# Kernel tuning notes

Hardware: AMD Instinct MI355X
Metric: run time of the kernel (lower is better)

Reference implementation:

```python
import jax, jax.numpy as jnp
import numpy as np

BATCH, IN_DIM, HID, OUT_DIM = 8192, 128, 1024, 128
W_SCALE = 0.05  # keep tanh out of saturation, like xavier init


def setup_inputs() -> dict:
    key = jax.random.key(0)
    k = jax.random.split(key, 5)
    return {
        "u": jax.random.normal(k[0], (BATCH, IN_DIM), dtype=jnp.float32),
        "B_w": jax.random.normal(k[1], (HID, IN_DIM), dtype=jnp.float32) * W_SCALE,
        "Bs_full": jax.random.normal(k[2], (HID, HID), dtype=jnp.float32) * W_SCALE,
        "Ds_w": jax.random.normal(k[3], (OUT_DIM, HID), dtype=jnp.float32) * W_SCALE,
        "D_w": jax.random.normal(k[4], (OUT_DIM, IN_DIM), dtype=jnp.float32) * W_SCALE,
    }


def reference(u, B_w, Bs_full, Ds_w, D_w):
    # s_i = tanh( sum_{j<i} Bs[i,j] * s_j + (B u)_i ),  y = Ds s + D u
    H = Bs_full.shape[0]
    Bs = jnp.tril(Bs_full, k=-1)          # strictly lower triangular [H, H]
    Bu = u @ B_w.T                        # [B, H]
    s0 = jnp.zeros_like(Bu)               # state buffer; entries >= i are 0,
                                          # so using the full masked row of Bs
                                          # equals the j<i partial sum.

    def step(s, xs):
        row, bu_i, i = xs                 # row: [H], bu_i: [B], i: scalar
        s_i = jnp.tanh(s @ row + bu_i)    # [B]
        return s.at[:, i].set(s_i), None

    s, _ = jax.lax.scan(step, s0, (Bs, Bu.T, jnp.arange(H)))
    return s @ Ds_w.T + u @ D_w.T         # [B, OUT_DIM]
```

## Files before the change

### kernel.cpp

```cpp
#include <hip/hip_runtime.h>

typedef unsigned short u16;
typedef __attribute__((ext_vector_type(8))) short bfrag;
typedef __attribute__((ext_vector_type(4))) float f32x4;

#define SROW 1032

__device__ __forceinline__ u16 f2bf(float x) {
    unsigned int v = __float_as_uint(x);
    return (u16)((v + 0x7FFFu + ((v >> 16) & 1u)) >> 16);
}

__device__ __forceinline__ float fast_tanh(float x) {
    float e = __builtin_amdgcn_exp2f(x * 2.885390081777927f);
    return __builtin_fmaf(-2.0f, __builtin_amdgcn_rcpf(e + 1.0f), 1.0f);
}

__global__ void ren_prologue(const float* __restrict__ Bs, const float* __restrict__ Bw,
                             const float* __restrict__ Ds, const float* __restrict__ Dw,
                             u16* __restrict__ bs16, u16* __restrict__ bw16,
                             u16* __restrict__ ds16, u16* __restrict__ dw16,
                             float* __restrict__ diagT)
{
    const int g = blockIdx.x * 256 + threadIdx.x;
    if (g < 262144) {
        const int idx = g * 4;
        const int i = idx >> 10, j = idx & 1023;
        const float4 v = *reinterpret_cast<const float4*>(Bs + idx);
        u16 o[4];
        o[0] = (j + 0 < i) ? f2bf(v.x) : (u16)0;
        o[1] = (j + 1 < i) ? f2bf(v.y) : (u16)0;
        o[2] = (j + 2 < i) ? f2bf(v.z) : (u16)0;
        o[3] = (j + 3 < i) ? f2bf(v.w) : (u16)0;
        *reinterpret_cast<uint2*>(bs16 + idx) = *reinterpret_cast<const uint2*>(o);
    } else if (g < 294912) {
        const int idx = (g - 262144) * 4;
        const float4 v = *reinterpret_cast<const float4*>(Bw + idx);
        u16 o[4] = { f2bf(v.x), f2bf(v.y), f2bf(v.z), f2bf(v.w) };
        *reinterpret_cast<uint2*>(bw16 + idx) = *reinterpret_cast<const uint2*>(o);
    } else if (g < 327680) {
        const int idx = (g - 294912) * 4;
        const float4 v = *reinterpret_cast<const float4*>(Ds + idx);
        u16 o[4] = { f2bf(v.x), f2bf(v.y), f2bf(v.z), f2bf(v.w) };
        *reinterpret_cast<uint2*>(ds16 + idx) = *reinterpret_cast<const uint2*>(o);
    } else if (g < 331776) {
        const int idx = (g - 327680) * 4;
        const float4 v = *reinterpret_cast<const float4*>(Dw + idx);
        u16 o[4] = { f2bf(v.x), f2bf(v.y), f2bf(v.z), f2bf(v.w) };
        *reinterpret_cast<uint2*>(dw16 + idx) = *reinterpret_cast<const uint2*>(o);
    } else if (g < 339968) {
        const int lin0 = (g - 331776) * 4;
        #pragma unroll
        for (int t = 0; t < 4; ++t) {
            const int l = lin0 + t;
            const int bb = l >> 10, rem = l & 1023, i = rem >> 5, j = rem & 31;
            diagT[l] = (j > i) ? Bs[(size_t)(bb * 32 + j) * 1024 + (bb * 32 + i)] : 0.0f;
        }
    }
}

__global__ __launch_bounds__(192) void ren_main(
    const float* __restrict__ u,
    const u16* __restrict__ bs16, const u16* __restrict__ bw16,
    const u16* __restrict__ ds16, const u16* __restrict__ dw16,
    const float* __restrict__ diagT,
    float* __restrict__ out)
{
    __shared__ __align__(16) u16   sh_S[32 * SROW];
    __shared__ __align__(16) float sh_acc[32 * 36];
    __shared__ __align__(16) float sh_dT[2][1024];

    const int tid  = threadIdx.x;
    const int wave = tid >> 6;
    const int lane = tid & 63;
    const int mt   = wave;
    const int lr   = lane & 15;
    const int lk8  = (lane >> 4) << 3;
    const int row0 = blockIdx.x << 5;

    bfrag fu[4];
    f32x4 accA0, accA1;

    if (wave < 2) {
        const float* up = u + (size_t)(row0 + mt * 16 + lr) * 128 + lk8;
        #pragma unroll
        for (int kk = 0; kk < 4; ++kk) {
            float4 a = *reinterpret_cast<const float4*>(up + kk * 32);
            float4 c = *reinterpret_cast<const float4*>(up + kk * 32 + 4);
            bfrag f;
            f[0] = (short)f2bf(a.x); f[1] = (short)f2bf(a.y);
            f[2] = (short)f2bf(a.z); f[3] = (short)f2bf(a.w);
            f[4] = (short)f2bf(c.x); f[5] = (short)f2bf(c.y);
            f[6] = (short)f2bf(c.z); f[7] = (short)f2bf(c.w);
            fu[kk] = f;
        }
        {
            const float4* g = reinterpret_cast<const float4*>(diagT + tid * 8);
            float4 a = g[0], c = g[1];
            *reinterpret_cast<float4*>(&sh_dT[0][tid * 8])     = a;
            *reinterpret_cast<float4*>(&sh_dT[0][tid * 8 + 4]) = c;
        }
        accA0 = (f32x4){0.f,0.f,0.f,0.f}; accA1 = (f32x4){0.f,0.f,0.f,0.f};
        const u16* p0 = bw16 + (size_t)(lr)      * 128 + lk8;
        const u16* p1 = bw16 + (size_t)(16 + lr) * 128 + lk8;
        #pragma unroll
        for (int kk = 0; kk < 4; ++kk) {
            accA0 = __builtin_amdgcn_mfma_f32_16x16x32_bf16(fu[kk], *reinterpret_cast<const bfrag*>(p0 + kk * 32), accA0, 0, 0, 0);
            accA1 = __builtin_amdgcn_mfma_f32_16x16x32_bf16(fu[kk], *reinterpret_cast<const bfrag*>(p1 + kk * 32), accA1, 0, 0, 0);
        }
        const int m = (mt << 4) + ((lane >> 4) << 2);
        #pragma unroll
        for (int rr = 0; rr < 4; ++rr) {
            sh_acc[(m + rr) * 36 + lr]      = accA0[rr];
            sh_acc[(m + rr) * 36 + 16 + lr] = accA1[rr];
        }
    }
    __syncthreads();

    for (int b = 0; b < 32; ++b) {
        if (wave == 2) {
            if (lane < 32) {
                float part[32];
                const float* accr = sh_acc + lane * 36;
                #pragma unroll
                for (int q = 0; q < 8; ++q) {
                    float4 v = reinterpret_cast<const float4*>(accr)[q];
                    part[4*q+0] = v.x; part[4*q+1] = v.y; part[4*q+2] = v.z; part[4*q+3] = v.w;
                }
                const float4* dT4 = reinterpret_cast<const float4*>(&sh_dT[b & 1][0]);
                float4 wreg[3][8];
                #pragma unroll
                for (int q = 0; q < 8; ++q) wreg[0][q] = dT4[q];
                #pragma unroll
                for (int q = 0; q < 8; ++q) wreg[1][q] = dT4[8 + q];
                u16* srow = sh_S + lane * SROW + (b << 5);
                u16 sv[8];
                #pragma unroll
                for (int i = 0; i < 32; ++i) {
                    if (i + 2 < 32) {
                        #pragma unroll
                        for (int q = (i + 3) >> 2; q < 8; ++q)
                            wreg[(i + 2) % 3][q] = dT4[((i + 2) << 3) + q];
                    }
                    float s = fast_tanh(part[i]);
                    sv[i & 7] = (u16)((__float_as_uint(s) + 0x8000u) >> 16);
                    if ((i & 7) == 7) {
                        uint4 pk;
                        pk.x = (unsigned)sv[0] | ((unsigned)sv[1] << 16);
                        pk.y = (unsigned)sv[2] | ((unsigned)sv[3] << 16);
                        pk.z = (unsigned)sv[4] | ((unsigned)sv[5] << 16);
                        pk.w = (unsigned)sv[6] | ((unsigned)sv[7] << 16);
                        *reinterpret_cast<uint4*>(srow + ((i >> 3) << 3)) = pk;
                    }
                    #pragma unroll
                    for (int q = (i + 1) >> 2; q < 8; ++q) {
                        float4 w = wreg[i % 3][q];
                        part[4*q+0] = __builtin_fmaf(w.x, s, part[4*q+0]);
                        part[4*q+1] = __builtin_fmaf(w.y, s, part[4*q+1]);
                        part[4*q+2] = __builtin_fmaf(w.z, s, part[4*q+2]);
                        part[4*q+3] = __builtin_fmaf(w.w, s, part[4*q+3]);
                    }
                }
            }
        } else if (b < 31) {
            const int nb = b + 1;
            const float4* g = reinterpret_cast<const float4*>(diagT + (nb << 10) + tid * 8);
            float4 st0 = g[0], st1 = g[1];

            accA0 = (f32x4){0.f,0.f,0.f,0.f}; accA1 = (f32x4){0.f,0.f,0.f,0.f};
            const u16* p0 = bw16 + (size_t)((nb << 5) + lr)      * 128 + lk8;
            const u16* p1 = bw16 + (size_t)((nb << 5) + 16 + lr) * 128 + lk8;
            #pragma unroll
            for (int kk = 0; kk < 4; ++kk) {
                accA0 = __builtin_amdgcn_mfma_f32_16x16x32_bf16(fu[kk], *reinterpret_cast<const bfrag*>(p0 + kk * 32), accA0, 0, 0, 0);
                accA1 = __builtin_amdgcn_mfma_f32_16x16x32_bf16(fu[kk], *reinterpret_cast<const bfrag*>(p1 + kk * 32), accA1, 0, 0, 0);
            }
            const u16* bsp0 = bs16 + (size_t)((nb << 5) + lr)      * 1024 + lk8;
            const u16* bsp1 = bs16 + (size_t)((nb << 5) + 16 + lr) * 1024 + lk8;
            const u16* ssp  = sh_S + ((mt << 4) + lr) * SROW + lk8;
            #pragma unroll 8
            for (int kc = 0; kc < b; ++kc) {
                bfrag af = *reinterpret_cast<const bfrag*>(ssp + (kc << 5));
                accA0 = __builtin_amdgcn_mfma_f32_16x16x32_bf16(af, *reinterpret_cast<const bfrag*>(bsp0 + (kc << 5)), accA0, 0, 0, 0);
                accA1 = __builtin_amdgcn_mfma_f32_16x16x32_bf16(af, *reinterpret_cast<const bfrag*>(bsp1 + (kc << 5)), accA1, 0, 0, 0);
            }
            *reinterpret_cast<float4*>(&sh_dT[nb & 1][tid * 8])     = st0;
            *reinterpret_cast<float4*>(&sh_dT[nb & 1][tid * 8 + 4]) = st1;
        }
        __syncthreads();

        if (wave < 2 && b < 31) {
            const int nb = b + 1;
            const u16* bsp0 = bs16 + (size_t)((nb << 5) + lr)      * 1024 + lk8;
            const u16* bsp1 = bs16 + (size_t)((nb << 5) + 16 + lr) * 1024 + lk8;
            const u16* ssp  = sh_S + ((mt << 4) + lr) * SROW + lk8;
            bfrag af = *reinterpret_cast<const bfrag*>(ssp + (b << 5));
            accA0 = __builtin_amdgcn_mfma_f32_16x16x32_bf16(af, *reinterpret_cast<const bfrag*>(bsp0 + (b << 5)), accA0, 0, 0, 0);
            accA1 = __builtin_amdgcn_mfma_f32_16x16x32_bf16(af, *reinterpret_cast<const bfrag*>(bsp1 + (b << 5)), accA1, 0, 0, 0);
            const int m = (mt << 4) + ((lane >> 4) << 2);
            #pragma unroll
            for (int rr = 0; rr < 4; ++rr) {
                sh_acc[(m + rr) * 36 + lr]      = accA0[rr];
                sh_acc[(m + rr) * 36 + 16 + lr] = accA1[rr];
            }
        }
        __syncthreads();
    }

    if (wave >= 2) return;

    f32x4 ey[8];
    #pragma unroll
    for (int t = 0; t < 8; ++t) ey[t] = (f32x4){0.f,0.f,0.f,0.f};

    const u16* ssp = sh_S + ((mt << 4) + lr) * SROW + lk8;
    #pragma unroll 2
    for (int kc = 0; kc < 32; ++kc) {
        bfrag af = *reinterpret_cast<const bfrag*>(ssp + (kc << 5));
        #pragma unroll
        for (int t = 0; t < 8; ++t) {
            bfrag bf = *reinterpret_cast<const bfrag*>(ds16 + (size_t)(t * 16 + lr) * 1024 + (kc << 5) + lk8);
            ey[t] = __builtin_amdgcn_mfma_f32_16x16x32_bf16(af, bf, ey[t], 0, 0, 0);
        }
    }
    #pragma unroll
    for (int kk = 0; kk < 4; ++kk) {
        #pragma unroll
        for (int t = 0; t < 8; ++t) {
            bfrag bf = *reinterpret_cast<const bfrag*>(dw16 + (t * 16 + lr) * 128 + (kk << 5) + lk8);
            ey[t] = __builtin_amdgcn_mfma_f32_16x16x32_bf16(fu[kk], bf, ey[t], 0, 0, 0);
        }
    }
    {
        const int mbase = row0 + (mt << 4) + ((lane >> 4) << 2);
        #pragma unroll
        for (int t = 0; t < 8; ++t) {
            #pragma unroll
            for (int rr = 0; rr < 4; ++rr)
                out[(size_t)(mbase + rr) * 128 + t * 16 + lr] = ey[t][rr];
        }
    }
}

extern "C" void kernel_launch(void* const* d_in, const int* in_sizes, int n_in,
                              void* d_out, int out_size, void* d_ws, size_t ws_size,
                              hipStream_t stream)
{
    const float* u  = (const float*)d_in[0];
    const float* Bw = (const float*)d_in[1];
    const float* Bs = (const float*)d_in[2];
    const float* Ds = (const float*)d_in[3];
    const float* Dw = (const float*)d_in[4];
    float* out = (float*)d_out;

    u16* bs16 = (u16*)d_ws;
    u16* bw16 = bs16 + 1024 * 1024;
    u16* ds16 = bw16 + 1024 * 128;
    u16* dw16 = ds16 + 128 * 1024;
    float* diagT = (float*)(dw16 + 128 * 128);

    ren_prologue<<<1328, 256, 0, stream>>>(Bs, Bw, Ds, Dw, bs16, bw16, ds16, dw16, diagT);
    ren_main<<<256, 192, 0, stream>>>(u, bs16, bw16, ds16, dw16, diagT, out);
}
```

Measured before the change: 190.0 us.

## Halve recurrence block size to 16 and split serial tanh across two lane halves

The sequential block width drops from 32 to 16 (64 blocks), so each serial triangular solve step does half the dependent FMA chain, and the MFMA waves use one 16-wide tile per block. The serial wave now uses all 64 lanes: lanes 0-15 and 16-31 each run a duplicated pA/pB chain, and the selected result is written to sh_S with scalar stores. sh_S is zero-filled with one extra padding row for lanes beyond 32. The aim is to shorten the critical path of the recurrence, at the cost of twice as many barriers and block iterations and less MFMA work per sync.

```diff
diff --git a/kernel.cpp b/kernel.cpp
--- a/kernel.cpp
+++ b/kernel.cpp
@@ -5,6 +5,8 @@
 typedef __attribute__((ext_vector_type(4))) float f32x4;
 
 #define SROW 1032
+#define NBLK 64
+#define ACCW 20
 
 __device__ __forceinline__ u16 f2bf(float x) {
     unsigned int v = __float_as_uint(x);
@@ -48,13 +50,13 @@
         const float4 v = *reinterpret_cast<const float4*>(Dw + idx);
         u16 o[4] = { f2bf(v.x), f2bf(v.y), f2bf(v.z), f2bf(v.w) };
         *reinterpret_cast<uint2*>(dw16 + idx) = *reinterpret_cast<const uint2*>(o);
-    } else if (g < 339968) {
+    } else if (g < 335872) {
         const int lin0 = (g - 331776) * 4;
         #pragma unroll
         for (int t = 0; t < 4; ++t) {
             const int l = lin0 + t;
-            const int bb = l >> 10, rem = l & 1023, i = rem >> 5, j = rem & 31;
-            diagT[l] = (j > i) ? Bs[(size_t)(bb * 32 + j) * 1024 + (bb * 32 + i)] : 0.0f;
+            const int bb = l >> 8, rem = l & 255, i = rem >> 4, j = rem & 15;
+            diagT[l] = (j > i) ? Bs[(size_t)(bb * 16 + j) * 1024 + (bb * 16 + i)] : 0.0f;
         }
     }
 }
@@ -66,9 +68,9 @@
     const float* __restrict__ diagT,
     float* __restrict__ out)
 {
-    __shared__ __align__(16) u16   sh_S[32 * SROW];
-    __shared__ __align__(16) float sh_acc[32 * 36];
-    __shared__ __align__(16) float sh_dT[2][1024];
+    __shared__ __align__(16) u16   sh_S[33 * SROW];
+    __shared__ __align__(16) float sh_acc[32 * ACCW];
+    __shared__ __align__(16) float sh_dT[2][256];
 
     const int tid  = threadIdx.x;
     const int wave = tid >> 6;
@@ -78,8 +80,11 @@
     const int lk8  = (lane >> 4) << 3;
     const int row0 = blockIdx.x << 5;
 
+    for (int e = tid * 8; e < 33 * SROW; e += 192 * 8)
+        *reinterpret_cast<uint4*>(sh_S + e) = (uint4){0u, 0u, 0u, 0u};
+
     bfrag fu[4];
-    f32x4 accA0, accA1;
+    f32x4 acc;
 
     if (wave < 2) {
         const float* up = u + (size_t)(row0 + mt * 16 + lr) * 128 + lk8;
@@ -94,115 +99,100 @@
             f[6] = (short)f2bf(c.z); f[7] = (short)f2bf(c.w);
             fu[kk] = f;
         }
-        {
-            const float4* g = reinterpret_cast<const float4*>(diagT + tid * 8);
-            float4 a = g[0], c = g[1];
-            *reinterpret_cast<float4*>(&sh_dT[0][tid * 8])     = a;
-            *reinterpret_cast<float4*>(&sh_dT[0][tid * 8 + 4]) = c;
-        }
-        accA0 = (f32x4){0.f,0.f,0.f,0.f}; accA1 = (f32x4){0.f,0.f,0.f,0.f};
-        const u16* p0 = bw16 + (size_t)(lr)      * 128 + lk8;
-        const u16* p1 = bw16 + (size_t)(16 + lr) * 128 + lk8;
-        #pragma unroll
-        for (int kk = 0; kk < 4; ++kk) {
-            accA0 = __builtin_amdgcn_mfma_f32_16x16x32_bf16(fu[kk], *reinterpret_cast<const bfrag*>(p0 + kk * 32), accA0, 0, 0, 0);
-            accA1 = __builtin_amdgcn_mfma_f32_16x16x32_bf16(fu[kk], *reinterpret_cast<const bfrag*>(p1 + kk * 32), accA1, 0, 0, 0);
-        }
+        if (tid < 128) {
+            float2 d0 = reinterpret_cast<const float2*>(diagT)[tid];
+            reinterpret_cast<float2*>(&sh_dT[0][0])[tid] = d0;
+        }
+        acc = (f32x4){0.f, 0.f, 0.f, 0.f};
+        const u16* p0 = bw16 + (size_t)lr * 128 + lk8;
+        #pragma unroll
+        for (int kk = 0; kk < 4; ++kk)
+            acc = __builtin_amdgcn_mfma_f32_16x16x32_bf16(fu[kk], *reinterpret_cast<const bfrag*>(p0 + kk * 32), acc, 0, 0, 0);
         const int m = (mt << 4) + ((lane >> 4) << 2);
         #pragma unroll
-        for (int rr = 0; rr < 4; ++rr) {
-            sh_acc[(m + rr) * 36 + lr]      = accA0[rr];
-            sh_acc[(m + rr) * 36 + 16 + lr] = accA1[rr];
-        }
+        for (int rr = 0; rr < 4; ++rr)
+            sh_acc[(m + rr) * ACCW + lr] = acc[rr];
     }
     __syncthreads();
 
-    for (int b = 0; b < 32; ++b) {
+    for (int b = 0; b < NBLK; ++b) {
         if (wave == 2) {
-            if (lane < 32) {
-                float part[32];
-                const float* accr = sh_acc + lane * 36;
+            const float* accr = sh_acc + (lane & 31) * ACCW;
+            float pA[16], pB[16];
+            #pragma unroll
+            for (int q = 0; q < 4; ++q) {
+                float4 v = reinterpret_cast<const float4*>(accr)[q];
+                pA[4*q+0] = v.x; pA[4*q+1] = v.y; pA[4*q+2] = v.z; pA[4*q+3] = v.w;
+                pB[4*q+0] = v.x; pB[4*q+1] = v.y; pB[4*q+2] = v.z; pB[4*q+3] = v.w;
+            }
+            const float4* dT4 = reinterpret_cast<const float4*>(&sh_dT[b & 1][0]);
+            float4 wreg[3][4];
+            #pragma unroll
+            for (int q = 0; q < 4; ++q) wreg[0][q] = dT4[q];
+            #pragma unroll
+            for (int q = 0; q < 4; ++q) wreg[1][q] = dT4[4 + q];
+            const bool isA = (lane < 16);
+            u16* srow = sh_S + min(lane, 32) * SROW + (b << 4);
+            #pragma unroll
+            for (int i = 0; i < 16; ++i) {
+                if (i + 2 < 16) {
+                    #pragma unroll
+                    for (int q = (i + 3) >> 2; q < 4; ++q)
+                        wreg[(i + 2) % 3][q] = dT4[((i + 2) << 2) + q];
+                }
+                float sA = fast_tanh(pA[i]);
+                float sB = fast_tanh(pB[i]);
+                float ss = isA ? sA : sB;
+                srow[i] = (u16)((__float_as_uint(ss) + 0x8000u) >> 16);
                 #pragma unroll
-                for (int q = 0; q < 8; ++q) {
-                    float4 v = reinterpret_cast<const float4*>(accr)[q];
-                    part[4*q+0] = v.x; part[4*q+1] = v.y; part[4*q+2] = v.z; part[4*q+3] = v.w;
-                }
-                const float4* dT4 = reinterpret_cast<const float4*>(&sh_dT[b & 1][0]);
-                float4 wreg[3][8];
-                #pragma unroll
-                for (int q = 0; q < 8; ++q) wreg[0][q] = dT4[q];
-                #pragma unroll
-                for (int q = 0; q < 8; ++q) wreg[1][q] = dT4[8 + q];
-                u16* srow = sh_S + lane * SROW + (b << 5);
-                u16 sv[8];
-                #pragma unroll
-                for (int i = 0; i < 32; ++i) {
-                    if (i + 2 < 32) {
-                        #pragma unroll
-                        for (int q = (i + 3) >> 2; q < 8; ++q)
-                            wreg[(i + 2) % 3][q] = dT4[((i + 2) << 3) + q];
-                    }
-                    float s = fast_tanh(part[i]);
-                    sv[i & 7] = (u16)((__float_as_uint(s) + 0x8000u) >> 16);
-                    if ((i & 7) == 7) {
-                        uint4 pk;
-                        pk.x = (unsigned)sv[0] | ((unsigned)sv[1] << 16);
-                        pk.y = (unsigned)sv[2] | ((unsigned)sv[3] << 16);
-                        pk.z = (unsigned)sv[4] | ((unsigned)sv[5] << 16);
-                        pk.w = (unsigned)sv[6] | ((unsigned)sv[7] << 16);
-                        *reinterpret_cast<uint4*>(srow + ((i >> 3) << 3)) = pk;
-                    }
-                    #pragma unroll
-                    for (int q = (i + 1) >> 2; q < 8; ++q) {
-                        float4 w = wreg[i % 3][q];
-                        part[4*q+0] = __builtin_fmaf(w.x, s, part[4*q+0]);
-                        part[4*q+1] = __builtin_fmaf(w.y, s, part[4*q+1]);
-                        part[4*q+2] = __builtin_fmaf(w.z, s, part[4*q+2]);
-                        part[4*q+3] = __builtin_fmaf(w.w, s, part[4*q+3]);
-                    }
+                for (int q = (i + 1) >> 2; q < 4; ++q) {
+                    float4 w = wreg[i % 3][q];
+                    pA[4*q+0] = __builtin_fmaf(w.x, sA, pA[4*q+0]);
+                    pA[4*q+1] = __builtin_fmaf(w.y, sA, pA[4*q+1]);
+                    pA[4*q+2] = __builtin_fmaf(w.z, sA, pA[4*q+2]);
+                    pA[4*q+3] = __builtin_fmaf(w.w, sA, pA[4*q+3]);
+                    pB[4*q+0] = __builtin_fmaf(w.x, sB, pB[4*q+0]);
+                    pB[4*q+1] = __builtin_fmaf(w.y, sB, pB[4*q+1]);
+                    pB[4*q+2] = __builtin_fmaf(w.z, sB, pB[4*q+2]);
+                    pB[4*q+3] = __builtin_fmaf(w.w, sB, pB[4*q+3]);
                 }
             }
-        } else if (b < 31) {
-            const int nb = b + 1;
-            const float4* g = reinterpret_cast<const float4*>(diagT + (nb << 10) + tid * 8);
-            float4 st0 = g[0], st1 = g[1];
-
-            accA0 = (f32x4){0.f,0.f,0.f,0.f}; accA1 = (f32x4){0.f,0.f,0.f,0.f};
-            const u16* p0 = bw16 + (size_t)((nb << 5) + lr)      * 128 + lk8;
-            const u16* p1 = bw16 + (size_t)((nb << 5) + 16 + lr) * 128 + lk8;
-            #pragma unroll
-            for (int kk = 0; kk < 4; ++kk) {
-                accA0 = __builtin_amdgcn_mfma_f32_16x16x32_bf16(fu[kk], *reinterpret_cast<const bfrag*>(p0 + kk * 32), accA0, 0, 0, 0);
-                accA1 = __builtin_amdgcn_mfma_f32_16x16x32_bf16(fu[kk], *reinterpret_cast<const bfrag*>(p1 + kk * 32), accA1, 0, 0, 0);
+        }
+
+        bfrag bfin;
+        const int nb = b + 1;
+        const int tf = b >> 1;
+        if (wave < 2 && b < NBLK - 1) {
+            float2 dstage;
+            if (tid < 128) dstage = reinterpret_cast<const float2*>(diagT + (nb << 8))[tid];
+            bfin = *reinterpret_cast<const bfrag*>(bs16 + (size_t)((nb << 4) + lr) * 1024 + (tf << 5) + lk8);
+
+            acc = (f32x4){0.f, 0.f, 0.f, 0.f};
+            const u16* p0 = bw16 + (size_t)((nb << 4) + lr) * 128 + lk8;
+            #pragma unroll
+            for (int kk = 0; kk < 4; ++kk)
+                acc = __builtin_amdgcn_mfma_f32_16x16x32_bf16(fu[kk], *reinterpret_cast<const bfrag*>(p0 + kk * 32), acc, 0, 0, 0);
+
+            const u16* bsp = bs16 + (size_t)((nb << 4) + lr) * 1024 + lk8;
+            const u16* ssp = sh_S + ((mt << 4) + lr) * SROW + lk8;
+            const int npart = b >> 1;
+            #pragma unroll 8
+            for (int t = 0; t < npart; ++t) {
+                bfrag af = *reinterpret_cast<const bfrag*>(ssp + (t << 5));
+                acc = __builtin_amdgcn_mfma_f32_16x16x32_bf16(af, *reinterpret_cast<const bfrag*>(bsp + (t << 5)), acc, 0, 0, 0);
             }
-            const u16* bsp0 = bs16 + (size_t)((nb << 5) + lr)      * 1024 + lk8;
-            const u16* bsp1 = bs16 + (size_t)((nb << 5) + 16 + lr) * 1024 + lk8;
-            const u16* ssp  = sh_S + ((mt << 4) + lr) * SROW + lk8;
-            #pragma unroll 8
-            for (int kc = 0; kc < b; ++kc) {
-                bfrag af = *reinterpret_cast<const bfrag*>(ssp + (kc << 5));
-                accA0 = __builtin_amdgcn_mfma_f32_16x16x32_bf16(af, *reinterpret_cast<const bfrag*>(bsp0 + (kc << 5)), accA0, 0, 0, 0);
-                accA1 = __builtin_amdgcn_mfma_f32_16x16x32_bf16(af, *reinterpret_cast<const bfrag*>(bsp1 + (kc << 5)), accA1, 0, 0, 0);
-            }
-            *reinterpret_cast<float4*>(&sh_dT[nb & 1][tid * 8])     = st0;
-            *reinterpret_cast<float4*>(&sh_dT[nb & 1][tid * 8 + 4]) = st1;
+            if (tid < 128) reinterpret_cast<float2*>(&sh_dT[nb & 1][0])[tid] = dstage;
         }
         __syncthreads();
 
-        if (wave < 2 && b < 31) {
-            const int nb = b + 1;
-            const u16* bsp0 = bs16 + (size_t)((nb << 5) + lr)      * 1024 + lk8;
-            const u16* bsp1 = bs16 + (size_t)((nb << 5) + 16 + lr) * 1024 + lk8;
-            const u16* ssp  = sh_S + ((mt << 4) + lr) * SROW + lk8;
-            bfrag af = *reinterpret_cast<const bfrag*>(ssp + (b << 5));
-            accA0 = __builtin_amdgcn_mfma_f32_16x16x32_bf16(af, *reinterpret_cast<const bfrag*>(bsp0 + (b << 5)), accA0, 0, 0, 0);
-            accA1 = __builtin_amdgcn_mfma_f32_16x16x32_bf16(af, *reinterpret_cast<const bfrag*>(bsp1 + (b << 5)), accA1, 0, 0, 0);
+        if (wave < 2 && b < NBLK - 1) {
+            const u16* ssp = sh_S + ((mt << 4) + lr) * SROW + lk8;
+            bfrag af = *reinterpret_cast<const bfrag*>(ssp + (tf << 5));
+            acc = __builtin_amdgcn_mfma_f32_16x16x32_bf16(af, bfin, acc, 0, 0, 0);
             const int m = (mt << 4) + ((lane >> 4) << 2);
             #pragma unroll
-            for (int rr = 0; rr < 4; ++rr) {
-                sh_acc[(m + rr) * 36 + lr]      = accA0[rr];
-                sh_acc[(m + rr) * 36 + 16 + lr] = accA1[rr];
-            }
+            for (int rr = 0; rr < 4; ++rr)
+                sh_acc[(m + rr) * ACCW + lr] = acc[rr];
         }
         __syncthreads();
     }
@@ -211,7 +201,7 @@
 
     f32x4 ey[8];
     #pragma unroll
-    for (int t = 0; t < 8; ++t) ey[t] = (f32x4){0.f,0.f,0.f,0.f};
+    for (int t = 0; t < 8; ++t) ey[t] = (f32x4){0.f, 0.f, 0.f, 0.f};
 
     const u16* ssp = sh_S + ((mt << 4) + lr) * SROW + lk8;
     #pragma unroll 2
@@ -259,6 +249,6 @@
     u16* dw16 = ds16 + 128 * 1024;
     float* diagT = (float*)(dw16 + 128 * 128);
 
-    ren_prologue<<<1328, 256, 0, stream>>>(Bs, Bw, Ds, Dw, bs16, bw16, ds16, dw16, diagT);
+    ren_prologue<<<1312, 256, 0, stream>>>(Bs, Bw, Ds, Dw, bs16, bw16, ds16, dw16, diagT);
     ren_main<<<256, 192, 0, stream>>>(u, bs16, bw16, ds16, dw16, diagT, out);
 }
```

Result: slower. 257.5 us (+35.5%).

## Collapse ren_main to single-wave blocks of 16 rows, removing barriers

Applied to the files above, without the earlier changes.

The 3-wave block (two MFMA waves plus one scalar tanh-recurrence wave over 32 rows) becomes one 64-lane wave that handles 16 rows, with 512 blocks instead of 256. The same wave does the serial within-block recurrence and then the MFMA accumulation for the next block, so all __syncthreads go away and the grid gets more, smaller blocks. In exchange, the recurrence and the MFMA work no longer overlap inside a block and only 16 lanes are active during the scalar phase. Overlap now has to come from several resident blocks per CU, which the smaller LDS footprint should allow.

```diff
diff --git a/kernel.cpp b/kernel.cpp
--- a/kernel.cpp
+++ b/kernel.cpp
@@ -5,6 +5,7 @@
 typedef __attribute__((ext_vector_type(4))) float f32x4;
 
 #define SROW 1032
+#define ACCW 36
 
 __device__ __forceinline__ u16 f2bf(float x) {
     unsigned int v = __float_as_uint(x);
@@ -59,30 +60,25 @@
     }
 }
 
-__global__ __launch_bounds__(192) void ren_main(
+__global__ __launch_bounds__(64) void ren_main(
     const float* __restrict__ u,
     const u16* __restrict__ bs16, const u16* __restrict__ bw16,
     const u16* __restrict__ ds16, const u16* __restrict__ dw16,
     const float* __restrict__ diagT,
     float* __restrict__ out)
 {
-    __shared__ __align__(16) u16   sh_S[32 * SROW];
-    __shared__ __align__(16) float sh_acc[32 * 36];
+    __shared__ __align__(16) u16   sh_S[16 * SROW];
+    __shared__ __align__(16) float sh_acc[16 * ACCW];
     __shared__ __align__(16) float sh_dT[2][1024];
 
-    const int tid  = threadIdx.x;
-    const int wave = tid >> 6;
-    const int lane = tid & 63;
-    const int mt   = wave;
+    const int lane = threadIdx.x;
     const int lr   = lane & 15;
     const int lk8  = (lane >> 4) << 3;
-    const int row0 = blockIdx.x << 5;
+    const int row0 = blockIdx.x << 4;
 
     bfrag fu[4];
-    f32x4 accA0, accA1;
-
-    if (wave < 2) {
-        const float* up = u + (size_t)(row0 + mt * 16 + lr) * 128 + lk8;
+    {
+        const float* up = u + (size_t)(row0 + lr) * 128 + lk8;
         #pragma unroll
         for (int kk = 0; kk < 4; ++kk) {
             float4 a = *reinterpret_cast<const float4*>(up + kk * 32);
@@ -94,126 +90,133 @@
             f[6] = (short)f2bf(c.z); f[7] = (short)f2bf(c.w);
             fu[kk] = f;
         }
-        {
-            const float4* g = reinterpret_cast<const float4*>(diagT + tid * 8);
-            float4 a = g[0], c = g[1];
-            *reinterpret_cast<float4*>(&sh_dT[0][tid * 8])     = a;
-            *reinterpret_cast<float4*>(&sh_dT[0][tid * 8 + 4]) = c;
-        }
-        accA0 = (f32x4){0.f,0.f,0.f,0.f}; accA1 = (f32x4){0.f,0.f,0.f,0.f};
-        const u16* p0 = bw16 + (size_t)(lr)      * 128 + lk8;
+    }
+
+    float4 st[4];
+    f32x4 acc0, acc1;
+    float part[32];
+
+    {
+        const float4* g = reinterpret_cast<const float4*>(diagT);
+        #pragma unroll
+        for (int t = 0; t < 4; ++t) st[t] = g[4 * lane + t];
+        float4* dd = reinterpret_cast<float4*>(&sh_dT[0][0]);
+        #pragma unroll
+        for (int t = 0; t < 4; ++t) dd[4 * lane + t] = st[t];
+
+        acc0 = (f32x4){0.f,0.f,0.f,0.f}; acc1 = (f32x4){0.f,0.f,0.f,0.f};
+        const u16* p0 = bw16 + (size_t)lr * 128 + lk8;
         const u16* p1 = bw16 + (size_t)(16 + lr) * 128 + lk8;
         #pragma unroll
         for (int kk = 0; kk < 4; ++kk) {
-            accA0 = __builtin_amdgcn_mfma_f32_16x16x32_bf16(fu[kk], *reinterpret_cast<const bfrag*>(p0 + kk * 32), accA0, 0, 0, 0);
-            accA1 = __builtin_amdgcn_mfma_f32_16x16x32_bf16(fu[kk], *reinterpret_cast<const bfrag*>(p1 + kk * 32), accA1, 0, 0, 0);
-        }
-        const int m = (mt << 4) + ((lane >> 4) << 2);
+            acc0 = __builtin_amdgcn_mfma_f32_16x16x32_bf16(fu[kk], *reinterpret_cast<const bfrag*>(p0 + kk * 32), acc0, 0, 0, 0);
+            acc1 = __builtin_amdgcn_mfma_f32_16x16x32_bf16(fu[kk], *reinterpret_cast<const bfrag*>(p1 + kk * 32), acc1, 0, 0, 0);
+        }
+        const int m = (lane >> 4) << 2;
         #pragma unroll
         for (int rr = 0; rr < 4; ++rr) {
-            sh_acc[(m + rr) * 36 + lr]      = accA0[rr];
-            sh_acc[(m + rr) * 36 + 16 + lr] = accA1[rr];
-        }
-    }
-    __syncthreads();
+            sh_acc[(m + rr) * ACCW + lr]      = acc0[rr];
+            sh_acc[(m + rr) * ACCW + 16 + lr] = acc1[rr];
+        }
+        if (lane < 16) {
+            const float4* ar = reinterpret_cast<const float4*>(sh_acc + lane * ACCW);
+            #pragma unroll
+            for (int q = 0; q < 8; ++q) {
+                float4 v = ar[q];
+                part[4*q+0] = v.x; part[4*q+1] = v.y; part[4*q+2] = v.z; part[4*q+3] = v.w;
+            }
+        }
+    }
 
     for (int b = 0; b < 32; ++b) {
-        if (wave == 2) {
-            if (lane < 32) {
-                float part[32];
-                const float* accr = sh_acc + lane * 36;
+        const int nb = b + 1;
+        if (nb < 32) {
+            const float4* g = reinterpret_cast<const float4*>(diagT + (nb << 10));
+            #pragma unroll
+            for (int t = 0; t < 4; ++t) st[t] = g[4 * lane + t];
+        }
+
+        if (lane < 16) {
+            const float4* dT4 = reinterpret_cast<const float4*>(&sh_dT[b & 1][0]);
+            float4 wreg[3][8];
+            #pragma unroll
+            for (int q = 0; q < 8; ++q) wreg[0][q] = dT4[q];
+            #pragma unroll
+            for (int q = 0; q < 8; ++q) wreg[1][q] = dT4[8 + q];
+            u16* srow = sh_S + lane * SROW + (b << 5);
+            u16 sv[8];
+            #pragma unroll
+            for (int i = 0; i < 32; ++i) {
+                if (i + 2 < 32) {
+                    #pragma unroll
+                    for (int q = (i + 3) >> 2; q < 8; ++q)
+                        wreg[(i + 2) % 3][q] = dT4[((i + 2) << 3) + q];
+                }
+                float s = fast_tanh(part[i]);
+                sv[i & 7] = (u16)((__float_as_uint(s) + 0x8000u) >> 16);
+                if ((i & 7) == 7) {
+                    uint4 pk;
+                    pk.x = (unsigned)sv[0] | ((unsigned)sv[1] << 16);
+                    pk.y = (unsigned)sv[2] | ((unsigned)sv[3] << 16);
+                    pk.z = (unsigned)sv[4] | ((unsigned)sv[5] << 16);
+                    pk.w = (unsigned)sv[6] | ((unsigned)sv[7] << 16);
+                    *reinterpret_cast<uint4*>(srow + ((i >> 3) << 3)) = pk;
+                }
+                #pragma unroll
+                for (int q = (i + 1) >> 2; q < 8; ++q) {
+                    float4 w = wreg[i % 3][q];
+                    part[4*q+0] = __builtin_fmaf(w.x, s, part[4*q+0]);
+                    part[4*q+1] = __builtin_fmaf(w.y, s, part[4*q+1]);
+                    part[4*q+2] = __builtin_fmaf(w.z, s, part[4*q+2]);
+                    part[4*q+3] = __builtin_fmaf(w.w, s, part[4*q+3]);
+                }
+            }
+        }
+
+        if (nb < 32) {
+            float4* dd = reinterpret_cast<float4*>(&sh_dT[nb & 1][0]);
+            #pragma unroll
+            for (int t = 0; t < 4; ++t) dd[4 * lane + t] = st[t];
+
+            acc0 = (f32x4){0.f,0.f,0.f,0.f}; acc1 = (f32x4){0.f,0.f,0.f,0.f};
+            const u16* q0 = bw16 + (size_t)((nb << 5) + lr) * 128 + lk8;
+            const u16* q1 = bw16 + (size_t)((nb << 5) + 16 + lr) * 128 + lk8;
+            #pragma unroll
+            for (int kk = 0; kk < 4; ++kk) {
+                acc0 = __builtin_amdgcn_mfma_f32_16x16x32_bf16(fu[kk], *reinterpret_cast<const bfrag*>(q0 + kk * 32), acc0, 0, 0, 0);
+                acc1 = __builtin_amdgcn_mfma_f32_16x16x32_bf16(fu[kk], *reinterpret_cast<const bfrag*>(q1 + kk * 32), acc1, 0, 0, 0);
+            }
+            const u16* bsp0 = bs16 + (size_t)((nb << 5) + lr) * 1024 + lk8;
+            const u16* bsp1 = bs16 + (size_t)((nb << 5) + 16 + lr) * 1024 + lk8;
+            const u16* ssp  = sh_S + lr * SROW + lk8;
+            #pragma unroll 8
+            for (int kc = 0; kc <= b; ++kc) {
+                bfrag af = *reinterpret_cast<const bfrag*>(ssp + (kc << 5));
+                acc0 = __builtin_amdgcn_mfma_f32_16x16x32_bf16(af, *reinterpret_cast<const bfrag*>(bsp0 + (kc << 5)), acc0, 0, 0, 0);
+                acc1 = __builtin_amdgcn_mfma_f32_16x16x32_bf16(af, *reinterpret_cast<const bfrag*>(bsp1 + (kc << 5)), acc1, 0, 0, 0);
+            }
+            const int m = (lane >> 4) << 2;
+            #pragma unroll
+            for (int rr = 0; rr < 4; ++rr) {
+                sh_acc[(m + rr) * ACCW + lr]      = acc0[rr];
+                sh_acc[(m + rr) * ACCW + 16 + lr] = acc1[rr];
+            }
+            if (lane < 16) {
+                const float4* ar = reinterpret_cast<const float4*>(sh_acc + lane * ACCW);
                 #pragma unroll
                 for (int q = 0; q < 8; ++q) {
-                    float4 v = reinterpret_cast<const float4*>(accr)[q];
+                    float4 v = ar[q];
                     part[4*q+0] = v.x; part[4*q+1] = v.y; part[4*q+2] = v.z; part[4*q+3] = v.w;
                 }
-                const float4* dT4 = reinterpret_cast<const float4*>(&sh_dT[b & 1][0]);
-                float4 wreg[3][8];
-                #pragma unroll
-                for (int q = 0; q < 8; ++q) wreg[0][q] = dT4[q];
-                #pragma unroll
-                for (int q = 0; q < 8; ++q) wreg[1][q] = dT4[8 + q];
-                u16* srow = sh_S + lane * SROW + (b << 5);
-                u16 sv[8];
-                #pragma unroll
-                for (int i = 0; i < 32; ++i) {
-                    if (i + 2 < 32) {
-                        #pragma unroll
-                        for (int q = (i + 3) >> 2; q < 8; ++q)
-                            wreg[(i + 2) % 3][q] = dT4[((i + 2) << 3) + q];
-                    }
-                    float s = fast_tanh(part[i]);
-                    sv[i & 7] = (u16)((__float_as_uint(s) + 0x8000u) >> 16);
-                    if ((i & 7) == 7) {
-                        uint4 pk;
-                        pk.x = (unsigned)sv[0] | ((unsigned)sv[1] << 16);
-                        pk.y = (unsigned)sv[2] | ((unsigned)sv[3] << 16);
-                        pk.z = (unsigned)sv[4] | ((unsigned)sv[5] << 16);
-                        pk.w = (unsigned)sv[6] | ((unsigned)sv[7] << 16);
-                        *reinterpret_cast<uint4*>(srow + ((i >> 3) << 3)) = pk;
-                    }
-                    #pragma unroll
-                    for (int q = (i + 1) >> 2; q < 8; ++q) {
-                        float4 w = wreg[i % 3][q];
-                        part[4*q+0] = __builtin_fmaf(w.x, s, part[4*q+0]);
-                        part[4*q+1] = __builtin_fmaf(w.y, s, part[4*q+1]);
-                        part[4*q+2] = __builtin_fmaf(w.z, s, part[4*q+2]);
-                        part[4*q+3] = __builtin_fmaf(w.w, s, part[4*q+3]);
-                    }
-                }
-            }
-        } else if (b < 31) {
-            const int nb = b + 1;
-            const float4* g = reinterpret_cast<const float4*>(diagT + (nb << 10) + tid * 8);
-            float4 st0 = g[0], st1 = g[1];
-
-            accA0 = (f32x4){0.f,0.f,0.f,0.f}; accA1 = (f32x4){0.f,0.f,0.f,0.f};
-            const u16* p0 = bw16 + (size_t)((nb << 5) + lr)      * 128 + lk8;
-            const u16* p1 = bw16 + (size_t)((nb << 5) + 16 + lr) * 128 + lk8;
-            #pragma unroll
-            for (int kk = 0; kk < 4; ++kk) {
-                accA0 = __builtin_amdgcn_mfma_f32_16x16x32_bf16(fu[kk], *reinterpret_cast<const bfrag*>(p0 + kk * 32), accA0, 0, 0, 0);
-                accA1 = __builtin_amdgcn_mfma_f32_16x16x32_bf16(fu[kk], *reinterpret_cast<const bfrag*>(p1 + kk * 32), accA1, 0, 0, 0);
-            }
-            const u16* bsp0 = bs16 + (size_t)((nb << 5) + lr)      * 1024 + lk8;
-            const u16* bsp1 = bs16 + (size_t)((nb << 5) + 16 + lr) * 1024 + lk8;
-            const u16* ssp  = sh_S + ((mt << 4) + lr) * SROW + lk8;
-            #pragma unroll 8
-            for (int kc = 0; kc < b; ++kc) {
-                bfrag af = *reinterpret_cast<const bfrag*>(ssp + (kc << 5));
-                accA0 = __builtin_amdgcn_mfma_f32_16x16x32_bf16(af, *reinterpret_cast<const bfrag*>(bsp0 + (kc << 5)), accA0, 0, 0, 0);
-                accA1 = __builtin_amdgcn_mfma_f32_16x16x32_bf16(af, *reinterpret_cast<const bfrag*>(bsp1 + (kc << 5)), accA1, 0, 0, 0);
-            }
-            *reinterpret_cast<float4*>(&sh_dT[nb & 1][tid * 8])     = st0;
-            *reinterpret_cast<float4*>(&sh_dT[nb & 1][tid * 8 + 4]) = st1;
-        }
-        __syncthreads();
-
-        if (wave < 2 && b < 31) {
-            const int nb = b + 1;
-            const u16* bsp0 = bs16 + (size_t)((nb << 5) + lr)      * 1024 + lk8;
-            const u16* bsp1 = bs16 + (size_t)((nb << 5) + 16 + lr) * 1024 + lk8;
-            const u16* ssp  = sh_S + ((mt << 4) + lr) * SROW + lk8;
-            bfrag af = *reinterpret_cast<const bfrag*>(ssp + (b << 5));
-            accA0 = __builtin_amdgcn_mfma_f32_16x16x32_bf16(af, *reinterpret_cast<const bfrag*>(bsp0 + (b << 5)), accA0, 0, 0, 0);
-            accA1 = __builtin_amdgcn_mfma_f32_16x16x32_bf16(af, *reinterpret_cast<const bfrag*>(bsp1 + (b << 5)), accA1, 0, 0, 0);
-            const int m = (mt << 4) + ((lane >> 4) << 2);
-            #pragma unroll
-            for (int rr = 0; rr < 4; ++rr) {
-                sh_acc[(m + rr) * 36 + lr]      = accA0[rr];
-                sh_acc[(m + rr) * 36 + 16 + lr] = accA1[rr];
-            }
-        }
-        __syncthreads();
-    }
-
-    if (wave >= 2) return;
+            }
+        }
+    }
 
     f32x4 ey[8];
     #pragma unroll
     for (int t = 0; t < 8; ++t) ey[t] = (f32x4){0.f,0.f,0.f,0.f};
 
-    const u16* ssp = sh_S + ((mt << 4) + lr) * SROW + lk8;
+    const u16* ssp = sh_S + lr * SROW + lk8;
     #pragma unroll 2
     for (int kc = 0; kc < 32; ++kc) {
         bfrag af = *reinterpret_cast<const bfrag*>(ssp + (kc << 5));
@@ -232,7 +235,7 @@
         }
     }
     {
-        const int mbase = row0 + (mt << 4) + ((lane >> 4) << 2);
+        const int mbase = row0 + ((lane >> 4) << 2);
         #pragma unroll
         for (int t = 0; t < 8; ++t) {
             #pragma unroll
@@ -260,5 +263,5 @@
     float* diagT = (float*)(dw16 + 128 * 128);
 
     ren_prologue<<<1328, 256, 0, stream>>>(Bs, Bw, Ds, Dw, bs16, bw16, ds16, dw16, diagT);
-    ren_main<<<256, 192, 0, stream>>>(u, bs16, bw16, ds16, dw16, diagT, out);
-}
+    ren_main<<<512, 64, 0, stream>>>(u, bs16, bw16, ds16, dw16, diagT, out);
+}
```

Measured after the change: 235.1 us. 23.8% more time.

## Split MFMA work across four waves per tile and prefetch diagonal Bs fragment

Applied to the files above, without the earlier changes.

Each block now runs four MFMA waves plus one scalar wave instead of two plus one. Each MFMA wave owns a 16x16 quadrant (m-tile, n-tile) rather than a 16x32 strip, which halves the serial MFMA chain per wave in the off-diagonal accumulation, the Bu projection and the output projection. The diagonal Bs fragment for the post-barrier MFMA is loaded before the barrier so that global load leaves the critical path. Scheduling barriers are added in the scalar tanh recurrence to pin instruction order. In exchange the block uses more waves and registers, and each wave reissues the u fragment loads.

```diff
diff --git a/kernel.cpp b/kernel.cpp
--- a/kernel.cpp
+++ b/kernel.cpp
@@ -5,6 +5,7 @@
 typedef __attribute__((ext_vector_type(4))) float f32x4;
 
 #define SROW 1032
+#define ACCW 36
 
 __device__ __forceinline__ u16 f2bf(float x) {
     unsigned int v = __float_as_uint(x);
@@ -59,7 +60,7 @@
     }
 }
 
-__global__ __launch_bounds__(192) void ren_main(
+__global__ __launch_bounds__(320) void ren_main(
     const float* __restrict__ u,
     const u16* __restrict__ bs16, const u16* __restrict__ bw16,
     const u16* __restrict__ ds16, const u16* __restrict__ dw16,
@@ -67,21 +68,22 @@
     float* __restrict__ out)
 {
     __shared__ __align__(16) u16   sh_S[32 * SROW];
-    __shared__ __align__(16) float sh_acc[32 * 36];
+    __shared__ __align__(16) float sh_acc[32 * ACCW];
     __shared__ __align__(16) float sh_dT[2][1024];
 
     const int tid  = threadIdx.x;
     const int wave = tid >> 6;
     const int lane = tid & 63;
-    const int mt   = wave;
+    const int mt   = (wave >> 1) & 1;
+    const int nt   = wave & 1;
     const int lr   = lane & 15;
     const int lk8  = (lane >> 4) << 3;
     const int row0 = blockIdx.x << 5;
 
     bfrag fu[4];
-    f32x4 accA0, accA1;
-
-    if (wave < 2) {
+    f32x4 acc;
+
+    if (wave < 4) {
         const float* up = u + (size_t)(row0 + mt * 16 + lr) * 128 + lk8;
         #pragma unroll
         for (int kk = 0; kk < 4; ++kk) {
@@ -94,45 +96,44 @@
             f[6] = (short)f2bf(c.z); f[7] = (short)f2bf(c.w);
             fu[kk] = f;
         }
-        {
-            const float4* g = reinterpret_cast<const float4*>(diagT + tid * 8);
-            float4 a = g[0], c = g[1];
+        if (tid < 128) {
+            const float4* g = reinterpret_cast<const float4*>(diagT);
+            float4 a = g[2 * tid], c = g[2 * tid + 1];
             *reinterpret_cast<float4*>(&sh_dT[0][tid * 8])     = a;
             *reinterpret_cast<float4*>(&sh_dT[0][tid * 8 + 4]) = c;
         }
-        accA0 = (f32x4){0.f,0.f,0.f,0.f}; accA1 = (f32x4){0.f,0.f,0.f,0.f};
-        const u16* p0 = bw16 + (size_t)(lr)      * 128 + lk8;
-        const u16* p1 = bw16 + (size_t)(16 + lr) * 128 + lk8;
-        #pragma unroll
-        for (int kk = 0; kk < 4; ++kk) {
-            accA0 = __builtin_amdgcn_mfma_f32_16x16x32_bf16(fu[kk], *reinterpret_cast<const bfrag*>(p0 + kk * 32), accA0, 0, 0, 0);
-            accA1 = __builtin_amdgcn_mfma_f32_16x16x32_bf16(fu[kk], *reinterpret_cast<const bfrag*>(p1 + kk * 32), accA1, 0, 0, 0);
-        }
+        acc = (f32x4){0.f, 0.f, 0.f, 0.f};
+        const u16* p0 = bw16 + (size_t)((nt << 4) + lr) * 128 + lk8;
+        #pragma unroll
+        for (int kk = 0; kk < 4; ++kk)
+            acc = __builtin_amdgcn_mfma_f32_16x16x32_bf16(fu[kk], *reinterpret_cast<const bfrag*>(p0 + kk * 32), acc, 0, 0, 0);
         const int m = (mt << 4) + ((lane >> 4) << 2);
         #pragma unroll
-        for (int rr = 0; rr < 4; ++rr) {
-            sh_acc[(m + rr) * 36 + lr]      = accA0[rr];
-            sh_acc[(m + rr) * 36 + 16 + lr] = accA1[rr];
-        }
+        for (int rr = 0; rr < 4; ++rr)
+            sh_acc[(m + rr) * ACCW + (nt << 4) + lr] = acc[rr];
     }
     __syncthreads();
 
     for (int b = 0; b < 32; ++b) {
-        if (wave == 2) {
+        bfrag bfin;
+        const int nb = b + 1;
+
+        if (wave == 4) {
             if (lane < 32) {
+                const float4* dT4 = reinterpret_cast<const float4*>(&sh_dT[b & 1][0]);
+                float4 wreg[3][8];
+                #pragma unroll
+                for (int q = 0; q < 8; ++q) wreg[0][q] = dT4[q];
+                #pragma unroll
+                for (int q = 0; q < 8; ++q) wreg[1][q] = dT4[8 + q];
                 float part[32];
-                const float* accr = sh_acc + lane * 36;
+                const float* accr = sh_acc + lane * ACCW;
                 #pragma unroll
                 for (int q = 0; q < 8; ++q) {
                     float4 v = reinterpret_cast<const float4*>(accr)[q];
                     part[4*q+0] = v.x; part[4*q+1] = v.y; part[4*q+2] = v.z; part[4*q+3] = v.w;
                 }
-                const float4* dT4 = reinterpret_cast<const float4*>(&sh_dT[b & 1][0]);
-                float4 wreg[3][8];
-                #pragma unroll
-                for (int q = 0; q < 8; ++q) wreg[0][q] = dT4[q];
-                #pragma unroll
-                for (int q = 0; q < 8; ++q) wreg[1][q] = dT4[8 + q];
+                __builtin_amdgcn_sched_barrier(0);
                 u16* srow = sh_S + lane * SROW + (b << 5);
                 u16 sv[8];
                 #pragma unroll
@@ -142,6 +143,7 @@
                         for (int q = (i + 3) >> 2; q < 8; ++q)
                             wreg[(i + 2) % 3][q] = dT4[((i + 2) << 3) + q];
                     }
+                    __builtin_amdgcn_sched_barrier(0);
                     float s = fast_tanh(part[i]);
                     sv[i & 7] = (u16)((__float_as_uint(s) + 0x8000u) >> 16);
                     if ((i & 7) == 7) {
@@ -160,84 +162,85 @@
                         part[4*q+2] = __builtin_fmaf(w.z, s, part[4*q+2]);
                         part[4*q+3] = __builtin_fmaf(w.w, s, part[4*q+3]);
                     }
+                    __builtin_amdgcn_sched_barrier(0);
                 }
             }
         } else if (b < 31) {
-            const int nb = b + 1;
-            const float4* g = reinterpret_cast<const float4*>(diagT + (nb << 10) + tid * 8);
-            float4 st0 = g[0], st1 = g[1];
-
-            accA0 = (f32x4){0.f,0.f,0.f,0.f}; accA1 = (f32x4){0.f,0.f,0.f,0.f};
-            const u16* p0 = bw16 + (size_t)((nb << 5) + lr)      * 128 + lk8;
-            const u16* p1 = bw16 + (size_t)((nb << 5) + 16 + lr) * 128 + lk8;
+            float4 st0, st1;
+            const bool stager = (tid < 128);
+            if (stager) {
+                const float4* g = reinterpret_cast<const float4*>(diagT + (nb << 10));
+                st0 = g[2 * tid]; st1 = g[2 * tid + 1];
+            }
+            const int ng = (nb << 5) + (nt << 4) + lr;
+            bfin = *reinterpret_cast<const bfrag*>(bs16 + (size_t)ng * 1024 + (b << 5) + lk8);
+
+            acc = (f32x4){0.f, 0.f, 0.f, 0.f};
+            const u16* p0 = bw16 + (size_t)ng * 128 + lk8;
             #pragma unroll
-            for (int kk = 0; kk < 4; ++kk) {
-                accA0 = __builtin_amdgcn_mfma_f32_16x16x32_bf16(fu[kk], *reinterpret_cast<const bfrag*>(p0 + kk * 32), accA0, 0, 0, 0);
-                accA1 = __builtin_amdgcn_mfma_f32_16x16x32_bf16(fu[kk], *reinterpret_cast<const bfrag*>(p1 + kk * 32), accA1, 0, 0, 0);
-            }
-            const u16* bsp0 = bs16 + (size_t)((nb << 5) + lr)      * 1024 + lk8;
-            const u16* bsp1 = bs16 + (size_t)((nb << 5) + 16 + lr) * 1024 + lk8;
-            const u16* ssp  = sh_S + ((mt << 4) + lr) * SROW + lk8;
+            for (int kk = 0; kk < 4; ++kk)
+                acc = __builtin_amdgcn_mfma_f32_16x16x32_bf16(fu[kk], *reinterpret_cast<const bfrag*>(p0 + kk * 32), acc, 0, 0, 0);
+
+            const u16* bsp = bs16 + (size_t)ng * 1024 + lk8;
+            const u16* ssp = sh_S + ((mt << 4) + lr) * SROW + lk8;
             #pragma unroll 8
             for (int kc = 0; kc < b; ++kc) {
                 bfrag af = *reinterpret_cast<const bfrag*>(ssp + (kc << 5));
-                accA0 = __builtin_amdgcn_mfma_f32_16x16x32_bf16(af, *reinterpret_cast<const bfrag*>(bsp0 + (kc << 5)), accA0, 0, 0, 0);
-                accA1 = __builtin_amdgcn_mfma_f32_16x16x32_bf16(af, *reinterpret_cast<const bfrag*>(bsp1 + (kc << 5)), accA1, 0, 0, 0);
-            }
-            *reinterpret_cast<float4*>(&sh_dT[nb & 1][tid * 8])     = st0;
-            *reinterpret_cast<float4*>(&sh_dT[nb & 1][tid * 8 + 4]) = st1;
+                acc = __builtin_amdgcn_mfma_f32_16x16x32_bf16(af, *reinterpret_cast<const bfrag*>(bsp + (kc << 5)), acc, 0, 0, 0);
+            }
+            if (stager) {
+                *reinterpret_cast<float4*>(&sh_dT[nb & 1][tid * 8])     = st0;
+                *reinterpret_cast<float4*>(&sh_dT[nb & 1][tid * 8 + 4]) = st1;
+            }
         }
         __syncthreads();
 
-        if (wave < 2 && b < 31) {
-            const int nb = b + 1;
-            const u16* bsp0 = bs16 + (size_t)((nb << 5) + lr)      * 1024 + lk8;
-            const u16* bsp1 = bs16 + (size_t)((nb << 5) + 16 + lr) * 1024 + lk8;
-            const u16* ssp  = sh_S + ((mt << 4) + lr) * SROW + lk8;
+        if (wave < 4 && b < 31) {
+            const u16* ssp = sh_S + ((mt << 4) + lr) * SROW + lk8;
             bfrag af = *reinterpret_cast<const bfrag*>(ssp + (b << 5));
-            accA0 = __builtin_amdgcn_mfma_f32_16x16x32_bf16(af, *reinterpret_cast<const bfrag*>(bsp0 + (b << 5)), accA0, 0, 0, 0);
-            accA1 = __builtin_amdgcn_mfma_f32_16x16x32_bf16(af, *reinterpret_cast<const bfrag*>(bsp1 + (b << 5)), accA1, 0, 0, 0);
+            acc = __builtin_amdgcn_mfma_f32_16x16x32_bf16(af, bfin, acc, 0, 0, 0);
             const int m = (mt << 4) + ((lane >> 4) << 2);
             #pragma unroll
-            for (int rr = 0; rr < 4; ++rr) {
-                sh_acc[(m + rr) * 36 + lr]      = accA0[rr];
-                sh_acc[(m + rr) * 36 + 16 + lr] = accA1[rr];
-            }
+            for (int rr = 0; rr < 4; ++rr)
+                sh_acc[(m + rr) * ACCW + (nt << 4) + lr] = acc[rr];
         }
         __syncthreads();
     }
 
-    if (wave >= 2) return;
-
-    f32x4 ey[8];
+    if (wave >= 4) return;
+
+    f32x4 ey[4];
     #pragma unroll
-    for (int t = 0; t < 8; ++t) ey[t] = (f32x4){0.f,0.f,0.f,0.f};
+    for (int t = 0; t < 4; ++t) ey[t] = (f32x4){0.f, 0.f, 0.f, 0.f};
 
     const u16* ssp = sh_S + ((mt << 4) + lr) * SROW + lk8;
-    #pragma unroll 2
+    #pragma unroll 4
     for (int kc = 0; kc < 32; ++kc) {
         bfrag af = *reinterpret_cast<const bfrag*>(ssp + (kc << 5));
         #pragma unroll
-        for (int t = 0; t < 8; ++t) {
-            bfrag bf = *reinterpret_cast<const bfrag*>(ds16 + (size_t)(t * 16 + lr) * 1024 + (kc << 5) + lk8);
+        for (int t = 0; t < 4; ++t) {
+            const int n = ((nt << 2) + t) * 16 + lr;
+            bfrag bf = *reinterpret_cast<const bfrag*>(ds16 + (size_t)n * 1024 + (kc << 5) + lk8);
             ey[t] = __builtin_amdgcn_mfma_f32_16x16x32_bf16(af, bf, ey[t], 0, 0, 0);
         }
     }
     #pragma unroll
     for (int kk = 0; kk < 4; ++kk) {
         #pragma unroll
-        for (int t = 0; t < 8; ++t) {
-            bfrag bf = *reinterpret_cast<const bfrag*>(dw16 + (t * 16 + lr) * 128 + (kk << 5) + lk8);
+        for (int t = 0; t < 4; ++t) {
+            const int n = ((nt << 2) + t) * 16 + lr;
+            bfrag bf = *reinterpret_cast<const bfrag*>(dw16 + n * 128 + (kk << 5) + lk8);
             ey[t] = __builtin_amdgcn_mfma_f32_16x16x32_bf16(fu[kk], bf, ey[t], 0, 0, 0);
         }
     }
     {
         const int mbase = row0 + (mt << 4) + ((lane >> 4) << 2);
         #pragma unroll
-        for (int t = 0; t < 8; ++t) {
+        for (int t = 0; t < 4; ++t) {
+            const int n = ((nt << 2) + t) * 16 + lr;
             #pragma unroll
             for (int rr = 0; rr < 4; ++rr)
-                out[(size_t)(mbase + rr) * 128 + t * 16 + lr] = ey[t][rr];
+                out[(size_t)(mbase + rr) * 128 + n] = ey[t][rr];
         }
     }
 }
@@ -260,5 +263,5 @@
     float* diagT = (float*)(dw16 + 128 * 128);
 
     ren_prologue<<<1328, 256, 0, stream>>>(Bs, Bw, Ds, Dw, bs16, bw16, ds16, dw16, diagT);
-    ren_main<<<256, 192, 0, stream>>>(u, bs16, bw16, ds16, dw16, diagT, out);
-}
+    ren_main<<<256, 320, 0, stream>>>(u, bs16, bw16, ds16, dw16, diagT, out);
+}
```

Result: slower. 239.7 us (+26.2%).
